# Kernel optimization log

Hardware: AMD Instinct MI355X
Metric: run time of the kernel (lower is better)

Reference implementation:

```python
import jax, jax.numpy as jnp
import numpy as np

B, S, F, H = 2, 2048, 1024, 16
HD = F // H


def setup_inputs() -> dict:
    key = jax.random.key(0)
    ks = jax.random.split(key, 9)
    Q = jax.random.normal(ks[0], (B, S, F), dtype=jnp.float32)
    K = jax.random.normal(ks[1], (B, S, F), dtype=jnp.float32)
    V = jax.random.normal(ks[2], (B, S, F), dtype=jnp.float32)
    # additive pre-softmax causal mask: 0 on/below diagonal, -1e9 above
    causal = jnp.tril(jnp.ones((S, S), dtype=bool))
    mask_1 = jnp.where(causal, 0.0, -1e9).astype(jnp.float32)[None, None]
    # multiplicative post-softmax mask in [0,1)
    mask_2 = jax.random.uniform(ks[3], (1, 1, S, S), dtype=jnp.float32)
    scale = 1.0 / np.sqrt(F)
    W_q = jax.random.normal(ks[4], (F, F), dtype=jnp.float32) * scale
    W_k = jax.random.normal(ks[5], (F, F), dtype=jnp.float32) * scale
    W_v = jax.random.normal(ks[6], (F, F), dtype=jnp.float32) * scale
    W_o = jax.random.normal(ks[7], (F, F), dtype=jnp.float32) * scale
    return {"Q": Q, "K": K, "V": V, "mask_1": mask_1, "mask_2": mask_2,
            "W_q": W_q, "W_k": W_k, "W_v": W_v, "W_o": W_o}


def reference(Q, K, V, mask_1, mask_2, W_q, W_k, W_v, W_o):
    # Linear projections (no bias), split into heads: [B,S,F] -> [B,H,S,HD]
    def proj(x, W):
        return (x @ W.T).reshape(B, S, H, HD).transpose(0, 2, 1, 3)
    q, k, v = proj(Q, W_q), proj(K, W_k), proj(V, W_v)
    # scores [B,H,S,S], scaled by sqrt(head_size)
    scores = jnp.einsum('bhqd,bhkd->bhqk', q, k) / np.sqrt(HD)
    scores = scores + mask_1  # additive pre-softmax mask
    probs = jax.nn.softmax(scores, axis=-1) * mask_2  # multiplicative post-softmax mask
    out = jnp.einsum('bhqk,bhkd->bhqd', probs, v)
    out = out.transpose(0, 2, 1, 3).reshape(B, S, F)
    return out @ W_o.T
```

## Files before the change

### kernel.cpp

```cpp
#include <hip/hip_runtime.h>
#include <hip/hip_bf16.h>
#include <stdint.h>

typedef __bf16 bf16_t;
typedef __bf16 bf16x8 __attribute__((ext_vector_type(8)));
typedef __bf16 bf16x4v __attribute__((ext_vector_type(4)));
typedef float f32x4 __attribute__((ext_vector_type(4)));

#define GLDS16(g, l)                                                         \
  __builtin_amdgcn_global_load_lds(                                          \
      (const __attribute__((address_space(1))) void*)(g),                    \
      (__attribute__((address_space(3))) void*)(l), 16, 0, 0)

__device__ __forceinline__ f32x4 mfma16(bf16x8 a, bf16x8 b, f32x4 c) {
  return __builtin_amdgcn_mfma_f32_16x16x32_bf16(a, b, c, 0, 0, 0);
}

static constexpr int S = 2048, F = 1024, H = 16, HD = 64;

static constexpr size_t OFF_PA  = 4194304;
static constexpr size_t OFF_PB  = 8388608;
static constexpr size_t OFF_WQ  = 12582912;
static constexpr size_t OFF_WK  = 13631488;
static constexpr size_t OFF_WV  = 14680064;
static constexpr size_t OFF_WO  = 15728640;
static constexpr size_t OFF_QP  = 16777216;
static constexpr size_t OFF_KP  = 20971520;
static constexpr size_t OFF_VPT = 25165824;
static constexpr size_t OFF_M2  = 29360128;

__global__ void cvt_small(const float* __restrict__ m2, const float* __restrict__ w0,
                          const float* __restrict__ w1, const float* __restrict__ w2,
                          const float* __restrict__ w3, bf16_t* __restrict__ dm,
                          bf16_t* __restrict__ e0, bf16_t* __restrict__ e1,
                          bf16_t* __restrict__ e2, bf16_t* __restrict__ e3) {
  const float* s;
  bf16_t* d;
  size_t r;
  if (blockIdx.x < 2048) {
    int t = blockIdx.x * 256 + threadIdx.x;
    r = (size_t)t * 8;
    s = m2; d = dm;
  } else {
    int t = (blockIdx.x - 2048) * 256 + threadIdx.x;
    int a = t >> 17;
    r = (size_t)(t & 0x1FFFF) * 8;
    s = (a == 0) ? w0 : (a == 1) ? w1 : (a == 2) ? w2 : w3;
    d = (a == 0) ? e0 : (a == 1) ? e1 : (a == 2) ? e2 : e3;
  }
  const float4* sp = (const float4*)(s + r);
  float4 u = sp[0], v = sp[1];
  bf16x8 o;
  o[0] = (bf16_t)u.x; o[1] = (bf16_t)u.y; o[2] = (bf16_t)u.z; o[3] = (bf16_t)u.w;
  o[4] = (bf16_t)v.x; o[5] = (bf16_t)v.y; o[6] = (bf16_t)v.z; o[7] = (bf16_t)v.w;
  *(bf16x8*)(d + r) = o;
}

__device__ __forceinline__ void stage128x32(const bf16_t* __restrict__ g, int ld,
                                            bf16_t* lds, int wv, int ln) {
#pragma unroll
  for (int i = 0; i < 2; ++i) {
    int ch  = wv * 2 + i;
    int row = ch * 16 + (ln >> 2);
    int col = (ln & 3) * 8;
    GLDS16(g + (size_t)row * ld + col, lds + ch * 512);
  }
}

__device__ __forceinline__ void pack16(const float4& p0, const float4& p1,
                                       const float4& p2, const float4& p3,
                                       float qscl, bf16x8& w0, bf16x8& w1) {
  w0[0] = (bf16_t)(p0.x * qscl); w0[1] = (bf16_t)(p0.y * qscl);
  w0[2] = (bf16_t)(p0.z * qscl); w0[3] = (bf16_t)(p0.w * qscl);
  w0[4] = (bf16_t)(p1.x * qscl); w0[5] = (bf16_t)(p1.y * qscl);
  w0[6] = (bf16_t)(p1.z * qscl); w0[7] = (bf16_t)(p1.w * qscl);
  w1[0] = (bf16_t)(p2.x * qscl); w1[1] = (bf16_t)(p2.y * qscl);
  w1[2] = (bf16_t)(p2.z * qscl); w1[3] = (bf16_t)(p2.w * qscl);
  w1[4] = (bf16_t)(p3.x * qscl); w1[5] = (bf16_t)(p3.y * qscl);
  w1[6] = (bf16_t)(p3.z * qscl); w1[7] = (bf16_t)(p3.w * qscl);
}

__global__ __launch_bounds__(256, 2) void proj_gemm(
    const float* __restrict__ Qf, const float* __restrict__ Kf, const float* __restrict__ Vf,
    const bf16_t* __restrict__ Wq, const bf16_t* __restrict__ Wk, const bf16_t* __restrict__ Wv,
    bf16_t* __restrict__ qp, bf16_t* __restrict__ kp, bf16_t* __restrict__ vpT) {
  __shared__ bf16_t As[2][128 * 32];
  __shared__ bf16_t Bs[2][128 * 32];
  const int z = blockIdx.z;
  const float* A = (z == 0) ? Qf : (z == 1) ? Kf : Vf;
  const bf16_t* W = (z == 0) ? Wq : (z == 1) ? Wk : Wv;
  const int m0 = blockIdx.x * 128, n0 = blockIdx.y * 128;
  const int tid = threadIdx.x, wv = tid >> 6, ln = tid & 63;
  const int wr = wv >> 1, wc = wv & 1, lr = ln & 15, lg = ln >> 4;
  const int ar = tid >> 1, ac = (tid & 1) * 16;
  const float* ag = A + (size_t)(m0 + ar) * F + ac;
  f32x4 acc[4][4];
#pragma unroll
  for (int i = 0; i < 4; ++i)
#pragma unroll
    for (int j = 0; j < 4; ++j) acc[i][j] = (f32x4){0.f, 0.f, 0.f, 0.f};

  {
    float4 p0 = *(const float4*)(ag + 0), p1 = *(const float4*)(ag + 4);
    float4 p2 = *(const float4*)(ag + 8), p3 = *(const float4*)(ag + 12);
    stage128x32(W + (size_t)n0 * F, F, Bs[0], wv, ln);
    bf16x8 w0, w1;
    pack16(p0, p1, p2, p3, 1.0f, w0, w1);
    *(bf16x8*)&As[0][ar * 32 + ac] = w0;
    *(bf16x8*)&As[0][ar * 32 + ac + 8] = w1;
  }
  __syncthreads();

  for (int k0 = 0; k0 < F; k0 += 32) {
    const int cur = (k0 >> 5) & 1;
    const bool pre = (k0 + 32 < F);
    float4 p0, p1, p2, p3;
    if (pre) {
      const float* an = ag + k0 + 32;
      p0 = *(const float4*)(an + 0); p1 = *(const float4*)(an + 4);
      p2 = *(const float4*)(an + 8); p3 = *(const float4*)(an + 12);
      stage128x32(W + (size_t)n0 * F + k0 + 32, F, Bs[cur ^ 1], wv, ln);
    }
    bf16x8 af[4], bfr[4];
#pragma unroll
    for (int i = 0; i < 4; ++i)
      af[i] = *(const bf16x8*)&As[cur][(wr * 64 + i * 16 + lr) * 32 + lg * 8];
#pragma unroll
    for (int j = 0; j < 4; ++j)
      bfr[j] = *(const bf16x8*)&Bs[cur][(wc * 64 + j * 16 + lr) * 32 + lg * 8];
#pragma unroll
    for (int i = 0; i < 4; ++i)
#pragma unroll
      for (int j = 0; j < 4; ++j) acc[i][j] = mfma16(af[i], bfr[j], acc[i][j]);
    if (pre) {
      bf16x8 w0, w1;
      pack16(p0, p1, p2, p3, 1.0f, w0, w1);
      *(bf16x8*)&As[cur ^ 1][ar * 32 + ac] = w0;
      *(bf16x8*)&As[cur ^ 1][ar * 32 + ac + 8] = w1;
    }
    __syncthreads();
  }

  const int rbase = m0 + wr * 64, cbase = n0 + wc * 64;
  if (z < 2) {
    bf16_t* out = (z == 0) ? qp : kp;
    const float qscl = (z == 0) ? 0.18033688f : 1.0f;
#pragma unroll
    for (int i = 0; i < 4; ++i)
#pragma unroll
      for (int j = 0; j < 4; ++j) {
        int r0 = rbase + i * 16 + lg * 4;
        int c  = cbase + j * 16 + lr;
        int b = r0 >> 11, s = r0 & 2047, h = c >> 6, d = c & 63;
        size_t base = ((size_t)(b * H + h) * S + s) * HD + d;
#pragma unroll
        for (int reg = 0; reg < 4; ++reg)
          out[base + (size_t)reg * HD] = (bf16_t)(acc[i][j][reg] * qscl);
      }
  } else {
#pragma unroll
    for (int i = 0; i < 4; ++i)
#pragma unroll
      for (int j = 0; j < 4; ++j) {
        int r0 = rbase + i * 16 + lg * 4;
        int c  = cbase + j * 16 + lr;
        int b = r0 >> 11, s = r0 & 2047, h = c >> 6, d = c & 63;
        size_t base = ((size_t)(b * H + h) * HD + d) * S + s;
        bf16x4v pv;
#pragma unroll
        for (int reg = 0; reg < 4; ++reg) pv[reg] = (bf16_t)acc[i][j][reg];
        *(bf16x4v*)&vpT[base] = pv;
      }
  }
}

__global__ __launch_bounds__(256, 2) void out_gemm(
    const bf16_t* __restrict__ PA, const bf16_t* __restrict__ PB,
    const float* __restrict__ lA, const float* __restrict__ lB,
    const bf16_t* __restrict__ W, float* __restrict__ out) {
  __shared__ bf16_t As[2][128 * 32];
  __shared__ bf16_t Bs[2][128 * 32];
  const int m0 = blockIdx.x * 128, n0 = blockIdx.y * 128;
  const int tid = threadIdx.x, wv = tid >> 6, ln = tid & 63;
  const int wr = wv >> 1, wc = wv & 1, lr = ln & 15, lg = ln >> 4;
  const int ar = tid >> 1, ac = (tid & 1) * 16;
  const int row = m0 + ar, s = row & 2047, b = row >> 11;
  const bool hiS = (s >= 1024);
  f32x4 acc[4][4];
#pragma unroll
  for (int i = 0; i < 4; ++i)
#pragma unroll
    for (int j = 0; j < 4; ++j) acc[i][j] = (f32x4){0.f, 0.f, 0.f, 0.f};

  {
    size_t pb0 = ((size_t)(b * 16) * S + s) * HD + ac;
    bf16x8 a0 = *(const bf16x8*)&PA[pb0];
    bf16x8 a1 = *(const bf16x8*)&PA[pb0 + 8];
    float lv = lA[(b * 16) * S + s], lw = 0.f;
    float va[16];
#pragma unroll
    for (int e = 0; e < 8; ++e) { va[e] = (float)a0[e]; va[8 + e] = (float)a1[e]; }
    if (hiS) {
      bf16x8 b0 = *(const bf16x8*)&PB[pb0];
      bf16x8 b1 = *(const bf16x8*)&PB[pb0 + 8];
      lw = lB[(b * 16) * S + s];
#pragma unroll
      for (int e = 0; e < 8; ++e) { va[e] += (float)b0[e]; va[8 + e] += (float)b1[e]; }
    }
    stage128x32(W + (size_t)n0 * F, F, Bs[0], wv, ln);
    float inv = 1.0f / (lv + lw);
    bf16x8 w0, w1;
#pragma unroll
    for (int e = 0; e < 8; ++e) {
      w0[e] = (bf16_t)(va[e] * inv);
      w1[e] = (bf16_t)(va[8 + e] * inv);
    }
    *(bf16x8*)&As[0][ar * 32 + ac] = w0;
    *(bf16x8*)&As[0][ar * 32 + ac + 8] = w1;
  }
  __syncthreads();

  for (int k0 = 0; k0 < F; k0 += 32) {
    const int cur = (k0 >> 5) & 1;
    const bool pre = (k0 + 32 < F);
    bf16x8 a0, a1, pb0v, pb1v;
    float lv = 0.f, lw = 0.f;
    if (pre) {
      const int kn = k0 + 32, h = kn >> 6, d0 = (kn & 63) + ac;
      size_t pbase = ((size_t)(b * 16 + h) * S + s) * HD + d0;
      a0 = *(const bf16x8*)&PA[pbase];
      a1 = *(const bf16x8*)&PA[pbase + 8];
      lv = lA[(b * 16 + h) * S + s];
      if (hiS) {
        pb0v = *(const bf16x8*)&PB[pbase];
        pb1v = *(const bf16x8*)&PB[pbase + 8];
        lw = lB[(b * 16 + h) * S + s];
      }
      stage128x32(W + (size_t)n0 * F + kn, F, Bs[cur ^ 1], wv, ln);
    }
    bf16x8 af[4], bfr[4];
#pragma unroll
    for (int i = 0; i < 4; ++i)
      af[i] = *(const bf16x8*)&As[cur][(wr * 64 + i * 16 + lr) * 32 + lg * 8];
#pragma unroll
    for (int j = 0; j < 4; ++j)
      bfr[j] = *(const bf16x8*)&Bs[cur][(wc * 64 + j * 16 + lr) * 32 + lg * 8];
#pragma unroll
    for (int i = 0; i < 4; ++i)
#pragma unroll
      for (int j = 0; j < 4; ++j) acc[i][j] = mfma16(af[i], bfr[j], acc[i][j]);
    if (pre) {
      float va[16];
#pragma unroll
      for (int e = 0; e < 8; ++e) { va[e] = (float)a0[e]; va[8 + e] = (float)a1[e]; }
      if (hiS) {
#pragma unroll
        for (int e = 0; e < 8; ++e) { va[e] += (float)pb0v[e]; va[8 + e] += (float)pb1v[e]; }
      }
      float inv = 1.0f / (lv + lw);
      bf16x8 w0, w1;
#pragma unroll
      for (int e = 0; e < 8; ++e) {
        w0[e] = (bf16_t)(va[e] * inv);
        w1[e] = (bf16_t)(va[8 + e] * inv);
      }
      *(bf16x8*)&As[cur ^ 1][ar * 32 + ac] = w0;
      *(bf16x8*)&As[cur ^ 1][ar * 32 + ac + 8] = w1;
    }
    __syncthreads();
  }
#pragma unroll
  for (int i = 0; i < 4; ++i)
#pragma unroll
    for (int j = 0; j < 4; ++j) {
      int r0 = m0 + wr * 64 + i * 16 + lg * 4;
      int c  = n0 + wc * 64 + j * 16 + lr;
#pragma unroll
      for (int reg = 0; reg < 4; ++reg)
        out[(size_t)(r0 + reg) * F + c] = acc[i][j][reg];
    }
}

__global__ __launch_bounds__(256, 4) void flash(
    const bf16_t* __restrict__ qp, const bf16_t* __restrict__ kp,
    const bf16_t* __restrict__ vpT, const bf16_t* __restrict__ m2b,
    bf16_t* __restrict__ PA, bf16_t* __restrict__ PB,
    float* __restrict__ lA, float* __restrict__ lB) {
  __shared__ bf16_t Ks[2][64 * 64];
  __shared__ bf16_t Vs[2][64 * 64];
  __shared__ bf16_t Pl[4][16 * 64];
  const int ur = blockIdx.x >> 5, bh = blockIdx.x & 31;
  const int grp = ur / 3, rem = ur % 3;
  int qt, kvlo, kvhi;
  if (rem == 2) { qt = 15 - grp; kvlo = 0; kvhi = qt; }
  else {
    qt = 31 - grp;
    int half = (qt + 2) >> 1;
    if (rem == 0) { kvlo = 0; kvhi = half - 1; }
    else          { kvlo = half; kvhi = qt; }
  }
  bf16_t* __restrict__ PO = (rem == 1) ? PB : PA;
  float*  __restrict__ LO = (rem == 1) ? lB : lA;

  const int tid = threadIdx.x, wv = tid >> 6, ln = tid & 63;
  const int lr = ln & 15, lg = ln >> 4;
  const bf16_t* qb = qp + (size_t)bh * S * HD;
  const bf16_t* kb = kp + (size_t)bh * S * HD;
  const bf16_t* vb = vpT + (size_t)bh * HD * S;
  const int q0w = qt * 64 + wv * 16;
  const int qg  = q0w + lr;

  bf16x8 bq[2];
#pragma unroll
  for (int h2 = 0; h2 < 2; ++h2)
    bq[h2] = *(const bf16x8*)&qb[(size_t)qg * HD + h2 * 32 + lg * 8];

  float ls = 0.f;
  f32x4 accv[4];
#pragma unroll
  for (int n = 0; n < 4; ++n) accv[n] = (f32x4){0.f, 0.f, 0.f, 0.f};

  const int srow0 = ln >> 3, scc0 = ln & 7;
  const int pxor = lr & 7;

#pragma unroll
  for (int i = 0; i < 2; ++i) {
    int ch = wv * 2 + i;
    int row = ch * 8 + srow0;
    int scc = scc0 ^ (row & 7);
    GLDS16(kb + (size_t)(kvlo * 64 + row) * HD + scc * 8, Ks[0] + ch * 512);
    GLDS16(vb + (size_t)row * S + kvlo * 64 + scc * 8, Vs[0] + ch * 512);
  }
  __syncthreads();

  for (int kt = kvlo; kt <= kvhi; ++kt) {
    const int k0 = kt * 64;
    const int cur = (kt - kvlo) & 1;

    bf16x4v m2v[4];
#pragma unroll
    for (int c = 0; c < 4; ++c)
      m2v[c] = *(const bf16x4v*)&m2b[(size_t)qg * S + k0 + c * 16 + lg * 4];

    if (kt < kvhi) {
      const int kn = k0 + 64;
#pragma unroll
      for (int i = 0; i < 2; ++i) {
        int ch = wv * 2 + i;
        int row = ch * 8 + srow0;
        int scc = scc0 ^ (row & 7);
        GLDS16(kb + (size_t)(kn + row) * HD + scc * 8, Ks[cur ^ 1] + ch * 512);
        GLDS16(vb + (size_t)row * S + kn + scc * 8, Vs[cur ^ 1] + ch * 512);
      }
    }

    f32x4 st[4];
    __builtin_amdgcn_s_setprio(1);
#pragma unroll
    for (int c = 0; c < 4; ++c) {
      int kr = c * 16 + lr;
      int sw = kr & 7;
      bf16x8 ak0 = *(const bf16x8*)&Ks[cur][kr * 64 + ((lg ^ sw) * 8)];
      bf16x8 ak1 = *(const bf16x8*)&Ks[cur][kr * 64 + (((4 + lg) ^ sw) * 8)];
      f32x4 t = (f32x4){0.f, 0.f, 0.f, 0.f};
      t = mfma16(ak0, bq[0], t);
      t = mfma16(ak1, bq[1], t);
      st[c] = t;
    }
    __builtin_amdgcn_s_setprio(0);
    if (kt == qt) {
#pragma unroll
      for (int c = 0; c < 4; ++c)
#pragma unroll
        for (int r = 0; r < 4; ++r) {
          int kgl = k0 + c * 16 + lg * 4 + r;
          if (kgl > qg) st[c][r] = -1e30f;
        }
    }
#pragma unroll
    for (int c = 0; c < 4; ++c) {
      bf16x4v pw;
      float p0 = exp2f(st[c][0]), p1 = exp2f(st[c][1]);
      float p2 = exp2f(st[c][2]), p3 = exp2f(st[c][3]);
      ls += (p0 + p1) + (p2 + p3);
      pw[0] = (bf16_t)(p0 * (float)m2v[c][0]);
      pw[1] = (bf16_t)(p1 * (float)m2v[c][1]);
      pw[2] = (bf16_t)(p2 * (float)m2v[c][2]);
      pw[3] = (bf16_t)(p3 * (float)m2v[c][3]);
      int chunk = (2 * c + (lg >> 1)) ^ pxor;
      *(bf16x4v*)&Pl[wv][lr * 64 + chunk * 8 + (lg & 1) * 4] = pw;
    }
    __builtin_amdgcn_s_setprio(1);
#pragma unroll
    for (int kc = 0; kc < 2; ++kc) {
      int pchunk = (4 * kc + lg) ^ pxor;
      bf16x8 pb = *(const bf16x8*)&Pl[wv][lr * 64 + pchunk * 8];
#pragma unroll
      for (int n = 0; n < 4; ++n) {
        int dr = n * 16 + lr;
        int sw = dr & 7;
        bf16x8 av = *(const bf16x8*)&Vs[cur][dr * 64 + (((kc * 4 + lg) ^ sw) * 8)];
        accv[n] = mfma16(av, pb, accv[n]);
      }
    }
    __builtin_amdgcn_s_setprio(0);
    __syncthreads();
  }

  ls += __shfl_xor(ls, 16, 64);
  ls += __shfl_xor(ls, 32, 64);
  if (lg == 0) LO[bh * S + qg] = ls;
#pragma unroll
  for (int n = 0; n < 4; ++n) {
    bf16x4v ov;
#pragma unroll
    for (int r = 0; r < 4; ++r) ov[r] = (bf16_t)accv[n][r];
    *(bf16x4v*)&PO[((size_t)bh * S + qg) * HD + n * 16 + lg * 4] = ov;
  }
}

extern "C" void kernel_launch(void* const* d_in, const int* in_sizes, int n_in,
                              void* d_out, int out_size, void* d_ws, size_t ws_size,
                              hipStream_t stream) {
  (void)in_sizes; (void)n_in; (void)out_size; (void)ws_size;
  const float* Q  = (const float*)d_in[0];
  const float* K  = (const float*)d_in[1];
  const float* V  = (const float*)d_in[2];
  const float* M2 = (const float*)d_in[4];
  const float* Wq = (const float*)d_in[5];
  const float* Wk = (const float*)d_in[6];
  const float* Wv = (const float*)d_in[7];
  const float* Wo = (const float*)d_in[8];
  bf16_t* ws = (bf16_t*)d_ws;

  bf16_t *WqB = ws + OFF_WQ, *WkB = ws + OFF_WK, *WvB = ws + OFF_WV, *WoB = ws + OFF_WO;
  bf16_t *qpB = ws + OFF_QP, *kpB = ws + OFF_KP, *vpT = ws + OFF_VPT;
  bf16_t *m2b = ws + OFF_M2;
  bf16_t *PA = ws + OFF_PA, *PB = ws + OFF_PB;
  float  *lA = (float*)(ws + OFF_WQ), *lB = (float*)(ws + OFF_WK);

  cvt_small<<<4096, 256, 0, stream>>>(M2, Wq, Wk, Wv, Wo, m2b, WqB, WkB, WvB, WoB);
  proj_gemm<<<dim3(32, 8, 3), 256, 0, stream>>>(Q, K, V, WqB, WkB, WvB, qpB, kpB, vpT);
  flash<<<dim3(1536), 256, 0, stream>>>(qpB, kpB, vpT, m2b, PA, PB, lA, lB);
  out_gemm<<<dim3(32, 8), 256, 0, stream>>>(PA, PB, lA, lB, WoB, (float*)d_out);
}
```

Before: 158.3 us.

## Pre-convert Q/K/V to bf16 and read mask_2 as fp32 in flash

The conversion kernel now turns the fp32 Q, K and V activations to bf16 in workspace, so the projection GEMM can stage both operands through async global-to-LDS loads instead of loading fp32 into registers and packing by hand. The bf16 copy of mask_2 is dropped and the flash kernel reads the fp32 mask directly. The cost is an extra pass writing and rereading about 24 MB of bf16 activations, plus twice the mask bytes read inside the attention loop. Workspace regions are reused for the partial outputs.

```diff
diff --git a/kernel.cpp b/kernel.cpp
--- a/kernel.cpp
+++ b/kernel.cpp
@@ -18,8 +18,9 @@
 
 static constexpr int S = 2048, F = 1024, H = 16, HD = 64;
 
-static constexpr size_t OFF_PA  = 4194304;
-static constexpr size_t OFF_PB  = 8388608;
+static constexpr size_t OFF_QB  = 0;
+static constexpr size_t OFF_KB  = 4194304;
+static constexpr size_t OFF_VB  = 8388608;
 static constexpr size_t OFF_WQ  = 12582912;
 static constexpr size_t OFF_WK  = 13631488;
 static constexpr size_t OFF_WV  = 14680064;
@@ -27,22 +28,26 @@
 static constexpr size_t OFF_QP  = 16777216;
 static constexpr size_t OFF_KP  = 20971520;
 static constexpr size_t OFF_VPT = 25165824;
-static constexpr size_t OFF_M2  = 29360128;
-
-__global__ void cvt_small(const float* __restrict__ m2, const float* __restrict__ w0,
-                          const float* __restrict__ w1, const float* __restrict__ w2,
-                          const float* __restrict__ w3, bf16_t* __restrict__ dm,
-                          bf16_t* __restrict__ e0, bf16_t* __restrict__ e1,
-                          bf16_t* __restrict__ e2, bf16_t* __restrict__ e3) {
+
+__global__ void cvt_all(const float* __restrict__ s0, const float* __restrict__ s1,
+                        const float* __restrict__ s2,
+                        const float* __restrict__ w0, const float* __restrict__ w1,
+                        const float* __restrict__ w2, const float* __restrict__ w3,
+                        bf16_t* __restrict__ d0, bf16_t* __restrict__ d1,
+                        bf16_t* __restrict__ d2,
+                        bf16_t* __restrict__ e0, bf16_t* __restrict__ e1,
+                        bf16_t* __restrict__ e2, bf16_t* __restrict__ e3) {
   const float* s;
   bf16_t* d;
   size_t r;
-  if (blockIdx.x < 2048) {
+  if (blockIdx.x < 6144) {
     int t = blockIdx.x * 256 + threadIdx.x;
-    r = (size_t)t * 8;
-    s = m2; d = dm;
+    int a = t >> 19;
+    r = (size_t)(t & 0x7FFFF) * 8;
+    s = (a == 0) ? s0 : (a == 1) ? s1 : s2;
+    d = (a == 0) ? d0 : (a == 1) ? d1 : d2;
   } else {
-    int t = (blockIdx.x - 2048) * 256 + threadIdx.x;
+    int t = (blockIdx.x - 6144) * 256 + threadIdx.x;
     int a = t >> 17;
     r = (size_t)(t & 0x1FFFF) * 8;
     s = (a == 0) ? w0 : (a == 1) ? w1 : (a == 2) ? w2 : w3;
@@ -67,58 +72,32 @@
   }
 }
 
-__device__ __forceinline__ void pack16(const float4& p0, const float4& p1,
-                                       const float4& p2, const float4& p3,
-                                       float qscl, bf16x8& w0, bf16x8& w1) {
-  w0[0] = (bf16_t)(p0.x * qscl); w0[1] = (bf16_t)(p0.y * qscl);
-  w0[2] = (bf16_t)(p0.z * qscl); w0[3] = (bf16_t)(p0.w * qscl);
-  w0[4] = (bf16_t)(p1.x * qscl); w0[5] = (bf16_t)(p1.y * qscl);
-  w0[6] = (bf16_t)(p1.z * qscl); w0[7] = (bf16_t)(p1.w * qscl);
-  w1[0] = (bf16_t)(p2.x * qscl); w1[1] = (bf16_t)(p2.y * qscl);
-  w1[2] = (bf16_t)(p2.z * qscl); w1[3] = (bf16_t)(p2.w * qscl);
-  w1[4] = (bf16_t)(p3.x * qscl); w1[5] = (bf16_t)(p3.y * qscl);
-  w1[6] = (bf16_t)(p3.z * qscl); w1[7] = (bf16_t)(p3.w * qscl);
-}
-
 __global__ __launch_bounds__(256, 2) void proj_gemm(
-    const float* __restrict__ Qf, const float* __restrict__ Kf, const float* __restrict__ Vf,
+    const bf16_t* __restrict__ Qb, const bf16_t* __restrict__ Kb, const bf16_t* __restrict__ Vb,
     const bf16_t* __restrict__ Wq, const bf16_t* __restrict__ Wk, const bf16_t* __restrict__ Wv,
     bf16_t* __restrict__ qp, bf16_t* __restrict__ kp, bf16_t* __restrict__ vpT) {
   __shared__ bf16_t As[2][128 * 32];
   __shared__ bf16_t Bs[2][128 * 32];
   const int z = blockIdx.z;
-  const float* A = (z == 0) ? Qf : (z == 1) ? Kf : Vf;
+  const bf16_t* A = (z == 0) ? Qb : (z == 1) ? Kb : Vb;
   const bf16_t* W = (z == 0) ? Wq : (z == 1) ? Wk : Wv;
   const int m0 = blockIdx.x * 128, n0 = blockIdx.y * 128;
   const int tid = threadIdx.x, wv = tid >> 6, ln = tid & 63;
   const int wr = wv >> 1, wc = wv & 1, lr = ln & 15, lg = ln >> 4;
-  const int ar = tid >> 1, ac = (tid & 1) * 16;
-  const float* ag = A + (size_t)(m0 + ar) * F + ac;
   f32x4 acc[4][4];
 #pragma unroll
   for (int i = 0; i < 4; ++i)
 #pragma unroll
     for (int j = 0; j < 4; ++j) acc[i][j] = (f32x4){0.f, 0.f, 0.f, 0.f};
 
-  {
-    float4 p0 = *(const float4*)(ag + 0), p1 = *(const float4*)(ag + 4);
-    float4 p2 = *(const float4*)(ag + 8), p3 = *(const float4*)(ag + 12);
-    stage128x32(W + (size_t)n0 * F, F, Bs[0], wv, ln);
-    bf16x8 w0, w1;
-    pack16(p0, p1, p2, p3, 1.0f, w0, w1);
-    *(bf16x8*)&As[0][ar * 32 + ac] = w0;
-    *(bf16x8*)&As[0][ar * 32 + ac + 8] = w1;
-  }
+  stage128x32(A + (size_t)m0 * F, F, As[0], wv, ln);
+  stage128x32(W + (size_t)n0 * F, F, Bs[0], wv, ln);
   __syncthreads();
 
   for (int k0 = 0; k0 < F; k0 += 32) {
     const int cur = (k0 >> 5) & 1;
-    const bool pre = (k0 + 32 < F);
-    float4 p0, p1, p2, p3;
-    if (pre) {
-      const float* an = ag + k0 + 32;
-      p0 = *(const float4*)(an + 0); p1 = *(const float4*)(an + 4);
-      p2 = *(const float4*)(an + 8); p3 = *(const float4*)(an + 12);
+    if (k0 + 32 < F) {
+      stage128x32(A + (size_t)m0 * F + k0 + 32, F, As[cur ^ 1], wv, ln);
       stage128x32(W + (size_t)n0 * F + k0 + 32, F, Bs[cur ^ 1], wv, ln);
     }
     bf16x8 af[4], bfr[4];
@@ -132,12 +111,6 @@
     for (int i = 0; i < 4; ++i)
 #pragma unroll
       for (int j = 0; j < 4; ++j) acc[i][j] = mfma16(af[i], bfr[j], acc[i][j]);
-    if (pre) {
-      bf16x8 w0, w1;
-      pack16(p0, p1, p2, p3, 1.0f, w0, w1);
-      *(bf16x8*)&As[cur ^ 1][ar * 32 + ac] = w0;
-      *(bf16x8*)&As[cur ^ 1][ar * 32 + ac + 8] = w1;
-    }
     __syncthreads();
   }
 
@@ -283,7 +256,7 @@
 
 __global__ __launch_bounds__(256, 4) void flash(
     const bf16_t* __restrict__ qp, const bf16_t* __restrict__ kp,
-    const bf16_t* __restrict__ vpT, const bf16_t* __restrict__ m2b,
+    const bf16_t* __restrict__ vpT, const float* __restrict__ m2f,
     bf16_t* __restrict__ PA, bf16_t* __restrict__ PB,
     float* __restrict__ lA, float* __restrict__ lB) {
   __shared__ bf16_t Ks[2][64 * 64];
@@ -337,10 +310,10 @@
     const int k0 = kt * 64;
     const int cur = (kt - kvlo) & 1;
 
-    bf16x4v m2v[4];
+    float4 m2v[4];
 #pragma unroll
     for (int c = 0; c < 4; ++c)
-      m2v[c] = *(const bf16x4v*)&m2b[(size_t)qg * S + k0 + c * 16 + lg * 4];
+      m2v[c] = *(const float4*)&m2f[(size_t)qg * S + k0 + c * 16 + lg * 4];
 
     if (kt < kvhi) {
       const int kn = k0 + 64;
@@ -383,10 +356,10 @@
       float p0 = exp2f(st[c][0]), p1 = exp2f(st[c][1]);
       float p2 = exp2f(st[c][2]), p3 = exp2f(st[c][3]);
       ls += (p0 + p1) + (p2 + p3);
-      pw[0] = (bf16_t)(p0 * (float)m2v[c][0]);
-      pw[1] = (bf16_t)(p1 * (float)m2v[c][1]);
-      pw[2] = (bf16_t)(p2 * (float)m2v[c][2]);
-      pw[3] = (bf16_t)(p3 * (float)m2v[c][3]);
+      pw[0] = (bf16_t)(p0 * m2v[c].x);
+      pw[1] = (bf16_t)(p1 * m2v[c].y);
+      pw[2] = (bf16_t)(p2 * m2v[c].z);
+      pw[3] = (bf16_t)(p3 * m2v[c].w);
       int chunk = (2 * c + (lg >> 1)) ^ pxor;
       *(bf16x4v*)&Pl[wv][lr * 64 + chunk * 8 + (lg & 1) * 4] = pw;
     }
@@ -433,14 +406,15 @@
   const float* Wo = (const float*)d_in[8];
   bf16_t* ws = (bf16_t*)d_ws;
 
+  bf16_t *Qb = ws + OFF_QB, *Kb = ws + OFF_KB, *Vb = ws + OFF_VB;
   bf16_t *WqB = ws + OFF_WQ, *WkB = ws + OFF_WK, *WvB = ws + OFF_WV, *WoB = ws + OFF_WO;
   bf16_t *qpB = ws + OFF_QP, *kpB = ws + OFF_KP, *vpT = ws + OFF_VPT;
-  bf16_t *m2b = ws + OFF_M2;
-  bf16_t *PA = ws + OFF_PA, *PB = ws + OFF_PB;
+  bf16_t *PA = ws + OFF_KB, *PB = ws + OFF_VB;
   float  *lA = (float*)(ws + OFF_WQ), *lB = (float*)(ws + OFF_WK);
 
-  cvt_small<<<4096, 256, 0, stream>>>(M2, Wq, Wk, Wv, Wo, m2b, WqB, WkB, WvB, WoB);
-  proj_gemm<<<dim3(32, 8, 3), 256, 0, stream>>>(Q, K, V, WqB, WkB, WvB, qpB, kpB, vpT);
-  flash<<<dim3(1536), 256, 0, stream>>>(qpB, kpB, vpT, m2b, PA, PB, lA, lB);
+  cvt_all<<<8192, 256, 0, stream>>>(Q, K, V, Wq, Wk, Wv, Wo,
+                                    Qb, Kb, Vb, WqB, WkB, WvB, WoB);
+  proj_gemm<<<dim3(32, 8, 3), 256, 0, stream>>>(Qb, Kb, Vb, WqB, WkB, WvB, qpB, kpB, vpT);
+  flash<<<dim3(1536), 256, 0, stream>>>(qpB, kpB, vpT, M2, PA, PB, lA, lB);
   out_gemm<<<dim3(32, 8), 256, 0, stream>>>(PA, PB, lA, lB, WoB, (float*)d_out);
 }
```

Result: faster. 146.0 us (-7.8%).
